# Performance work log

Measured on AMD Instinct MI355X. Metric: run time of the kernel, lower is better.

## Reference

```python
import jax, jax.numpy as jnp
import numpy as np

N, E, K, H, F_IN, F_OUT, Q = 50000, 1600000, 4, 4, 32, 32, 1


def setup_inputs() -> dict:
    key = jax.random.key(0)
    ks = jax.random.split(key, 5)
    x = jax.random.normal(ks[0], (N, H, F_IN, Q), dtype=jnp.float32)
    edge_index = jax.random.randint(ks[1], (2, E), 0, N, dtype=jnp.int64)
    edge_weight = jax.random.uniform(ks[2], (E,), dtype=jnp.float32)
    stdv = 1.0 / np.sqrt(F_IN * K)
    weight = jax.random.uniform(ks[3], (K, H, F_IN, F_OUT), dtype=jnp.float32, minval=-stdv, maxval=stdv)
    bias = jax.random.uniform(ks[4], (F_OUT,), dtype=jnp.float32, minval=-stdv, maxval=stdv)
    return {"x": x, "edge_index": edge_index, "edge_weight": edge_weight, "weight": weight, "bias": bias}


def reference(x, edge_index, edge_weight, weight, bias):
    # x: (n, h, f, q); weight: (K, h, f, g); edge_index: (2, E)
    n = x.shape[0]
    row, col = edge_index[0], edge_index[1]
    # remove_self_loops: zero out self-loop edges (static shapes, same math)
    mask = row != col
    ew = jnp.where(mask, edge_weight, jnp.zeros((), x.dtype))
    deg = jax.ops.segment_sum(mask.astype(x.dtype), row, num_segments=n)
    dinv = jnp.where(deg > 0, deg ** -0.5, jnp.zeros((), x.dtype))
    lap = -dinv[row] * ew * dinv[col]  # (E,)

    def spmm(t):
        # out[row] += lap * t[col]; t: (n, h, f, q)
        return jax.ops.segment_sum(lap[:, None, None, None] * t[col], row, num_segments=n)

    Kk = weight.shape[0]
    Tx0 = x
    out = jnp.einsum('nhfq,hfg->ngq', Tx0, weight[0])
    Tx1 = spmm(Tx0)
    out = out + jnp.einsum('nhfq,hfg->ngq', Tx1, weight[1])
    for k in range(2, Kk):
        Tx2 = 2.0 * spmm(Tx1) - Tx0
        out = out + jnp.einsum('nhfq,hfg->ngq', Tx2, weight[k])
        Tx0, Tx1 = Tx1, Tx2
    out = out[:, None]  # (n, 1, g, q) per collapse_H unsqueeze
    out = out + bias.reshape(1, 1, -1, 1)
    return out
```

## Files before the change

### kernel.cpp

```cpp
#include <hip/hip_runtime.h>


#define FEAT 128
#define GOUT 32
#define SCB 256
#define WPB 8
#define CH 4096
#define WCAP 16384
#define CAP 12032
#define TROW 160

typedef unsigned int uint;
typedef unsigned short ushort;

__device__ __forceinline__ ushort f2bf(float f) {
    uint u = __float_as_uint(f);
    return (ushort)((u + 0x7fffu + ((u >> 16) & 1u)) >> 16);
}
__device__ __forceinline__ float bflo(uint u) { return __uint_as_float(u << 16); }
__device__ __forceinline__ float bfhi(uint u) { return __uint_as_float(u & 0xffff0000u); }
__device__ __forceinline__ int tidx(int i) { return i + ((i >> 4) << 2); }

__global__ __launch_bounds__(1024) void bin_kernel(
    const int* __restrict__ ei, const float* __restrict__ ew, int E,
    int* __restrict__ bucketCursor, uint2* __restrict__ staging) {
    __shared__ int hist[256];
    __shared__ int base[256];
    int e0 = blockIdx.x * CH;
    int e1 = min(e0 + CH, E);
    int t = threadIdx.x;
    if (t < 256) hist[t] = 0;
    __syncthreads();
    for (int e = e0 + t; e < e1; e += 1024) {
        int r = ei[e], c = ei[(size_t)E + e];
        if (r != c) atomicAdd(&hist[r >> 8], 1);
    }
    __syncthreads();
    if (t < 256) {
        int h = hist[t];
        if (h > 0) {
            int run = atomicAdd(&bucketCursor[t], h);
            base[t] = t * CAP + run;
        }
        hist[t] = 0;
    }
    __syncthreads();
    for (int e = e0 + t; e < e1; e += 1024) {
        int r = ei[e], c = ei[(size_t)E + e];
        if (r == c) continue;
        float w = ew[e];
        int bk = r >> 8;
        int j = atomicAdd(&hist[bk], 1);
        int idx = base[bk] + j;
        if (idx < (bk + 1) * CAP)
            staging[idx] = make_uint2(__float_as_uint(w), ((uint)c << 16) | (uint)(r & 255));
    }
}

__global__ __launch_bounds__(256) void bucket_count_kernel(
    const uint2* __restrict__ staging, const int* __restrict__ bucketCursor,
    int* __restrict__ cnt, int n) {
    __shared__ int hist[256];
    int b = blockIdx.x;
    int t = threadIdx.x;
    hist[t] = 0;
    __syncthreads();
    int nrec = bucketCursor[b];
    const uint2* src = staging + (size_t)b * CAP;
    for (int k = t; k < nrec; k += 256)
        atomicAdd(&hist[src[k].y & 255], 1);
    __syncthreads();
    int r = (b << 8) + t;
    if (r < n) cnt[r] = hist[t];
}

__global__ void scan1_kernel(const int* __restrict__ cnt, int* __restrict__ partial,
                             int* __restrict__ blockSums, float* __restrict__ dinv, int n) {
    __shared__ int buf[2][SCB];
    int t = threadIdx.x;
    int i = blockIdx.x * SCB + t;
    int v = (i < n) ? cnt[i] : 0;
    if (i < n) dinv[i] = (v > 0) ? rsqrtf((float)v) : 0.0f;
    buf[0][t] = v;
    __syncthreads();
    int src = 0;
    for (int off = 1; off < SCB; off <<= 1) {
        int d = src ^ 1;
        buf[d][t] = buf[src][t] + ((t >= off) ? buf[src][t - off] : 0);
        __syncthreads();
        src = d;
    }
    int incl = buf[src][t];
    if (i < n) partial[i] = incl - v;
    if (t == SCB - 1) blockSums[blockIdx.x] = incl;
}

__global__ void scan2_kernel(const int* __restrict__ blockSums, int* __restrict__ blockOffsets,
                             int nb, int* __restrict__ total_out) {
    __shared__ int buf[2][SCB];
    __shared__ int carry_s;
    if (threadIdx.x == 0) carry_s = 0;
    __syncthreads();
    for (int base = 0; base < nb; base += SCB) {
        int i = base + (int)threadIdx.x;
        int v = (i < nb) ? blockSums[i] : 0;
        buf[0][threadIdx.x] = v;
        __syncthreads();
        int src = 0;
        for (int off = 1; off < SCB; off <<= 1) {
            int d = src ^ 1;
            buf[d][threadIdx.x] = buf[src][threadIdx.x] +
                                  ((threadIdx.x >= (unsigned)off) ? buf[src][threadIdx.x - off] : 0);
            __syncthreads();
            src = d;
        }
        int incl = buf[src][threadIdx.x];
        int c = carry_s;
        if (i < nb) blockOffsets[i] = c + incl - v;
        __syncthreads();
        if (threadIdx.x == SCB - 1) carry_s = c + incl;
        __syncthreads();
    }
    if (threadIdx.x == 0) *total_out = carry_s;
}

__global__ void scan3_kernel(const int* __restrict__ partial, const int* __restrict__ blockOffsets,
                             int* __restrict__ offsets, int n) {
    int i = blockIdx.x * blockDim.x + threadIdx.x;
    if (i < n) offsets[i] = partial[i] + blockOffsets[i / SCB];
}

__global__ __launch_bounds__(256) void scatter_kernel(
    const uint2* __restrict__ staging, const int* __restrict__ bucketCursor,
    const int* __restrict__ offsets, const float* __restrict__ dinv,
    uint* __restrict__ csr, int n) {
    __shared__ uint win[WCAP];
    __shared__ int roff[256];
    __shared__ int rcur[256];
    __shared__ float dloc[256];
    int b = blockIdx.x;
    int r0 = b << 8;
    int nrows = min(256, n - r0);
    int t = threadIdx.x;
    if (t < nrows) {
        roff[t] = offsets[r0 + t];
        dloc[t] = dinv[r0 + t];
    }
    rcur[t] = 0;
    __syncthreads();
    int wbeg = roff[0];
    int nrec = bucketCursor[b];
    bool fit = (nrec <= WCAP);
    const uint2* src = staging + (size_t)b * CAP;
    for (int k = t; k < nrec; k += 256) {
        uint2 rec = src[k];
        int col = rec.y >> 16;
        int rl = rec.y & 255;
        float lap = -dloc[rl] * __uint_as_float(rec.x) * dinv[col];
        uint colap = ((uint)col << 16) | (uint)f2bf(lap);
        int pos = roff[rl] + atomicAdd(&rcur[rl], 1);
        if (fit) win[pos - wbeg] = colap;
        else csr[pos] = colap;
    }
    __syncthreads();
    if (fit)
        for (int k = t; k < nrec; k += 256) csr[wbeg + k] = win[k];
}

__global__ __launch_bounds__(256) void cvt_einsum0_kernel(
    const float* __restrict__ x, ushort* __restrict__ xb,
    const float* __restrict__ W0, const float* __restrict__ bias,
    float* __restrict__ out, int n) {
    __shared__ __align__(16) float4 sW4[FEAT * GOUT / 4];
    __shared__ __align__(16) float sT[8 * TROW];
    const float* sW = (const float*)sW4;
    int t = threadIdx.x;
    const float4* wsrc = (const float4*)W0;
    for (int idx = t; idx < FEAT * GOUT / 4; idx += 256) sW4[idx] = wsrc[idx];
    size_t gi = (size_t)blockIdx.x * (8 * FEAT) + (size_t)t * 4;
    float4 v = make_float4(0.f, 0.f, 0.f, 0.f);
    bool inb = gi < (size_t)n * FEAT;
    if (inb) {
        v = *(const float4*)(x + gi);
        ushort4 o;
        o.x = f2bf(v.x); o.y = f2bf(v.y); o.z = f2bf(v.z); o.w = f2bf(v.w);
        *(ushort4*)(xb + gi) = o;
    }
    int nl = t >> 5;
    int f0 = 4 * (t & 31);
    *(float4*)&sT[nl * TROW + tidx(f0)] = v;
    __syncthreads();
    int l32 = t & 31;
    int q = l32 & 7;
    int part = l32 >> 3;
    float4 a4 = make_float4(0.f, 0.f, 0.f, 0.f);
#pragma unroll
    for (int j = 0; j < 8; ++j) {
        float4 t4 = *(const float4*)&sT[nl * TROW + tidx(part * 32 + 4 * j)];
        const float* wv0 = &sW[(part * 32 + 4 * j) * GOUT + 4 * q];
        float4 w0 = *(const float4*)(wv0);
        float4 w1 = *(const float4*)(wv0 + GOUT);
        float4 w2 = *(const float4*)(wv0 + 2 * GOUT);
        float4 w3 = *(const float4*)(wv0 + 3 * GOUT);
        a4.x += t4.x * w0.x + t4.y * w1.x + t4.z * w2.x + t4.w * w3.x;
        a4.y += t4.x * w0.y + t4.y * w1.y + t4.z * w2.y + t4.w * w3.y;
        a4.z += t4.x * w0.z + t4.y * w1.z + t4.z * w2.z + t4.w * w3.z;
        a4.w += t4.x * w0.w + t4.y * w1.w + t4.z * w2.w + t4.w * w3.w;
    }
    a4.x += __shfl_down(a4.x, 8);  a4.y += __shfl_down(a4.y, 8);
    a4.z += __shfl_down(a4.z, 8);  a4.w += __shfl_down(a4.w, 8);
    a4.x += __shfl_down(a4.x, 16); a4.y += __shfl_down(a4.y, 16);
    a4.z += __shfl_down(a4.z, 16); a4.w += __shfl_down(a4.w, 16);
    int node = blockIdx.x * 8 + nl;
    if (part == 0 && node < n) {
        const float4 b4 = *(const float4*)(bias + 4 * q);
        float4 r;
        r.x = a4.x + b4.x; r.y = a4.y + b4.y; r.z = a4.z + b4.z; r.w = a4.w + b4.w;
        *(float4*)(out + (size_t)node * GOUT + 4 * q) = r;
    }
}

__global__ __launch_bounds__(512) void spmm_fused_kernel(
    const ushort* __restrict__ inb, const ushort* __restrict__ sub,
    ushort* __restrict__ outb, const int* __restrict__ offsets,
    const uint* __restrict__ csr, const float* __restrict__ Wk,
    float* __restrict__ out, int n, int has_sub) {
    __shared__ __align__(16) float4 sW4[FEAT * GOUT / 4];
    __shared__ __align__(16) float sT[WPB][TROW];
    const float* sW = (const float*)sW4;
    int w = threadIdx.x >> 6;
    int lane = threadIdx.x & 63;
    int node = blockIdx.x * WPB + w;
    const float4* wsrc = (const float4*)Wk;
    for (int idx = threadIdx.x; idx < FEAT * GOUT / 4; idx += 512) sW4[idx] = wsrc[idx];
    float ox = 0.f, oy = 0.f;
    if (node < n) {
        int beg = offsets[node], end = offsets[node + 1];
        float ax = 0.f, ay = 0.f;
        int j = beg;
        for (; j + 8 <= end; j += 8) {
            uint q[8], u[8];
#pragma unroll
            for (int k = 0; k < 8; ++k) q[k] = __builtin_nontemporal_load(csr + j + k);
#pragma unroll
            for (int k = 0; k < 8; ++k)
                u[k] = ((const uint*)(inb + (size_t)(q[k] >> 16) * FEAT))[lane];
#pragma unroll
            for (int k = 0; k < 8; ++k) {
                float l = bflo(q[k]);
                ax += l * bflo(u[k]);
                ay += l * bfhi(u[k]);
            }
        }
        for (; j < end; ++j) {
            uint qe = __builtin_nontemporal_load(csr + j);
            uint u = ((const uint*)(inb + (size_t)(qe >> 16) * FEAT))[lane];
            float l = bflo(qe);
            ax += l * bflo(u);
            ay += l * bfhi(u);
        }
        ox = ax; oy = ay;
        if (has_sub) {
            uint s = __builtin_nontemporal_load((const uint*)(sub + (size_t)node * FEAT) + lane);
            ox = 2.f * ax - bflo(s);
            oy = 2.f * ay - bfhi(s);
        }
        uint o = (uint)f2bf(ox) | ((uint)f2bf(oy) << 16);
        __builtin_nontemporal_store(o, (uint*)(outb + (size_t)node * FEAT) + lane);
    }
    *(float2*)&sT[w][tidx(2 * lane)] = make_float2(ox, oy);
    __syncthreads();
    int q = lane & 7;
    int part = lane >> 3;
    float4 a4 = make_float4(0.f, 0.f, 0.f, 0.f);
#pragma unroll
    for (int j = 0; j < 4; ++j) {
        float4 t4 = *(const float4*)&sT[w][20 * part + 4 * j];
        const float* wv0 = &sW[(part * 16 + 4 * j) * GOUT + 4 * q];
        float4 w0 = *(const float4*)(wv0);
        float4 w1 = *(const float4*)(wv0 + GOUT);
        float4 w2 = *(const float4*)(wv0 + 2 * GOUT);
        float4 w3 = *(const float4*)(wv0 + 3 * GOUT);
        a4.x += t4.x * w0.x + t4.y * w1.x + t4.z * w2.x + t4.w * w3.x;
        a4.y += t4.x * w0.y + t4.y * w1.y + t4.z * w2.y + t4.w * w3.y;
        a4.z += t4.x * w0.z + t4.y * w1.z + t4.z * w2.z + t4.w * w3.z;
        a4.w += t4.x * w0.w + t4.y * w1.w + t4.z * w2.w + t4.w * w3.w;
    }
#pragma unroll
    for (int off = 8; off < 64; off <<= 1) {
        a4.x += __shfl_down(a4.x, off);
        a4.y += __shfl_down(a4.y, off);
        a4.z += __shfl_down(a4.z, off);
        a4.w += __shfl_down(a4.w, off);
    }
    if (part == 0 && node < n) {
        float4* po = (float4*)(out + (size_t)node * GOUT + 4 * q);
        float4 cur = *po;
        cur.x += a4.x; cur.y += a4.y; cur.z += a4.z; cur.w += a4.w;
        *po = cur;
    }
}

extern "C" void kernel_launch(void* const* d_in, const int* in_sizes, int n_in,
                              void* d_out, int out_size, void* d_ws, size_t ws_size,
                              hipStream_t stream) {
    const float* x = (const float*)d_in[0];
    const int* ei = (const int*)d_in[1];
    const float* ew = (const float*)d_in[2];
    const float* W = (const float*)d_in[3];
    const float* bias = (const float*)d_in[4];
    float* out = (float*)d_out;

    const int N = in_sizes[0] / FEAT;
    const int E = in_sizes[1] / 2;
    const int NB = (N + SCB - 1) / SCB;
    const int NBUK = (N + 255) >> 8;

    char* p = (char*)d_ws;
    auto alloc = [&](size_t bytes) {
        char* q = p;
        p += (bytes + 255) & ~(size_t)255;
        return q;
    };
    int* cnt = (int*)alloc((size_t)N * 4);
    int* offsets = (int*)alloc(((size_t)N + 1) * 4);
    float* dinv = (float*)alloc((size_t)N * 4);
    int* partial = (int*)alloc((size_t)N * 4);
    int* blockSums = (int*)alloc((size_t)NB * 4);
    int* blockOffsets = (int*)alloc((size_t)NB * 4);
    int* bucketCursor = (int*)alloc((size_t)NBUK * 4);
    uint* csr = (uint*)alloc((size_t)E * 4);
    ushort* xb = (ushort*)alloc((size_t)N * FEAT * 2);
    ushort* Ab = (ushort*)alloc((size_t)N * FEAT * 2);
    ushort* Bb = (ushort*)alloc((size_t)N * FEAT * 2);
    uint2* staging = (uint2*)Ab;
    (void)ws_size;

    hipMemsetAsync(bucketCursor, 0, (size_t)NBUK * 4, stream);

    bin_kernel<<<(E + CH - 1) / CH, 1024, 0, stream>>>(ei, ew, E, bucketCursor, staging);
    bucket_count_kernel<<<NBUK, 256, 0, stream>>>(staging, bucketCursor, cnt, N);
    scan1_kernel<<<NB, SCB, 0, stream>>>(cnt, partial, blockSums, dinv, N);
    scan2_kernel<<<1, SCB, 0, stream>>>(blockSums, blockOffsets, NB, offsets + N);
    scan3_kernel<<<NB, SCB, 0, stream>>>(partial, blockOffsets, offsets, N);
    scatter_kernel<<<NBUK, 256, 0, stream>>>(staging, bucketCursor, offsets, dinv, csr, N);

    cvt_einsum0_kernel<<<(N + 7) / 8, 256, 0, stream>>>(x, xb, W, bias, out, N);

    int sg = (N + WPB - 1) / WPB;
    spmm_fused_kernel<<<sg, 512, 0, stream>>>(xb, nullptr, Ab, offsets, csr,
                                              W + 1 * FEAT * GOUT, out, N, 0);
    spmm_fused_kernel<<<sg, 512, 0, stream>>>(Ab, xb, Bb, offsets, csr,
                                              W + 2 * FEAT * GOUT, out, N, 1);
    spmm_fused_kernel<<<sg, 512, 0, stream>>>(Bb, Ab, Ab, offsets, csr,
                                              W + 3 * FEAT * GOUT, out, N, 1);
}
```

Baseline: 407.4 us.

## Split features into 32-wide chunks for SpMM with per-chunk einsum atomics

New measurement: 384.1 us. 1.06x faster.

```diff
diff --git a/kernel.cpp b/kernel.cpp
--- a/kernel.cpp
+++ b/kernel.cpp
@@ -3,8 +3,9 @@
 
 #define FEAT 128
 #define GOUT 32
+#define NCH 4
+#define CHF 32
 #define SCB 256
-#define WPB 8
 #define CH 4096
 #define WCAP 16384
 #define CAP 12032
@@ -177,17 +178,17 @@
     int t = threadIdx.x;
     const float4* wsrc = (const float4*)W0;
     for (int idx = t; idx < FEAT * GOUT / 4; idx += 256) sW4[idx] = wsrc[idx];
-    size_t gi = (size_t)blockIdx.x * (8 * FEAT) + (size_t)t * 4;
+    int node = blockIdx.x * 8 + (t >> 5);
+    int f0 = 4 * (t & 31);
     float4 v = make_float4(0.f, 0.f, 0.f, 0.f);
-    bool inb = gi < (size_t)n * FEAT;
-    if (inb) {
-        v = *(const float4*)(x + gi);
+    if (node < n) {
+        v = *(const float4*)(x + (size_t)node * FEAT + f0);
         ushort4 o;
         o.x = f2bf(v.x); o.y = f2bf(v.y); o.z = f2bf(v.z); o.w = f2bf(v.w);
-        *(ushort4*)(xb + gi) = o;
+        int j0 = f0 >> 5;
+        *(ushort4*)(xb + ((size_t)j0 * n + node) * CHF + (f0 & 31)) = o;
     }
     int nl = t >> 5;
-    int f0 = 4 * (t & 31);
     *(float4*)&sT[nl * TROW + tidx(f0)] = v;
     __syncthreads();
     int l32 = t & 31;
@@ -211,7 +212,6 @@
     a4.z += __shfl_down(a4.z, 8);  a4.w += __shfl_down(a4.w, 8);
     a4.x += __shfl_down(a4.x, 16); a4.y += __shfl_down(a4.y, 16);
     a4.z += __shfl_down(a4.z, 16); a4.w += __shfl_down(a4.w, 16);
-    int node = blockIdx.x * 8 + nl;
     if (part == 0 && node < n) {
         const float4 b4 = *(const float4*)(bias + 4 * q);
         float4 r;
@@ -220,84 +220,68 @@
     }
 }
 
-__global__ __launch_bounds__(512) void spmm_fused_kernel(
+__global__ __launch_bounds__(512) void spmm_chunk_kernel(
     const ushort* __restrict__ inb, const ushort* __restrict__ sub,
     ushort* __restrict__ outb, const int* __restrict__ offsets,
     const uint* __restrict__ csr, const float* __restrict__ Wk,
-    float* __restrict__ out, int n, int has_sub) {
-    __shared__ __align__(16) float4 sW4[FEAT * GOUT / 4];
-    __shared__ __align__(16) float sT[WPB][TROW];
-    const float* sW = (const float*)sW4;
-    int w = threadIdx.x >> 6;
-    int lane = threadIdx.x & 63;
-    int node = blockIdx.x * WPB + w;
-    const float4* wsrc = (const float4*)Wk;
-    for (int idx = threadIdx.x; idx < FEAT * GOUT / 4; idx += 512) sW4[idx] = wsrc[idx];
-    float ox = 0.f, oy = 0.f;
+    float* __restrict__ out, int n, int has_sub, int nbj) {
+    __shared__ __align__(16) float sW[CHF * GOUT];
+    __shared__ float sT2[8][4][CHF];
+    int j = blockIdx.x / nbj;
+    int b = blockIdx.x % nbj;
+    int t = threadIdx.x;
+    const float4* wsrc = (const float4*)(Wk + j * CHF * GOUT);
+    for (int i2 = t; i2 < CHF * GOUT / 4; i2 += 512) ((float4*)sW)[i2] = wsrc[i2];
+    int w = t >> 6, lane = t & 63, s = lane >> 4, u = lane & 15;
+    int node = b * 32 + w * 4 + s;
+    int beg = 0, deg = 0;
+    if (node < n) { beg = offsets[node]; deg = offsets[node + 1] - beg; }
+    int m = deg;
+    m = max(m, __shfl_xor(m, 16));
+    m = max(m, __shfl_xor(m, 32));
+    const uint* inb_u = (const uint*)inb;
+    size_t jbase = (size_t)j * n * 16;
+    float tax = 0.f, tay = 0.f;
+    for (int it = 0; it < m; it += 4) {
+        uint q[4], uu[4];
+#pragma unroll
+        for (int k = 0; k < 4; ++k) {
+            int idx = it + k;
+            q[k] = (idx < deg) ? csr[beg + idx] : 0u;
+        }
+#pragma unroll
+        for (int k = 0; k < 4; ++k)
+            uu[k] = inb_u[jbase + (size_t)(q[k] >> 16) * 16 + u];
+#pragma unroll
+        for (int k = 0; k < 4; ++k) {
+            float l = bflo(q[k]);
+            tax += l * bflo(uu[k]);
+            tay += l * bfhi(uu[k]);
+        }
+    }
+    float ox = tax, oy = tay;
     if (node < n) {
-        int beg = offsets[node], end = offsets[node + 1];
-        float ax = 0.f, ay = 0.f;
-        int j = beg;
-        for (; j + 8 <= end; j += 8) {
-            uint q[8], u[8];
-#pragma unroll
-            for (int k = 0; k < 8; ++k) q[k] = __builtin_nontemporal_load(csr + j + k);
-#pragma unroll
-            for (int k = 0; k < 8; ++k)
-                u[k] = ((const uint*)(inb + (size_t)(q[k] >> 16) * FEAT))[lane];
-#pragma unroll
-            for (int k = 0; k < 8; ++k) {
-                float l = bflo(q[k]);
-                ax += l * bflo(u[k]);
-                ay += l * bfhi(u[k]);
-            }
-        }
-        for (; j < end; ++j) {
-            uint qe = __builtin_nontemporal_load(csr + j);
-            uint u = ((const uint*)(inb + (size_t)(qe >> 16) * FEAT))[lane];
-            float l = bflo(qe);
-            ax += l * bflo(u);
-            ay += l * bfhi(u);
-        }
-        ox = ax; oy = ay;
+        size_t base = jbase + (size_t)node * 16 + u;
         if (has_sub) {
-            uint s = __builtin_nontemporal_load((const uint*)(sub + (size_t)node * FEAT) + lane);
-            ox = 2.f * ax - bflo(s);
-            oy = 2.f * ay - bfhi(s);
-        }
-        uint o = (uint)f2bf(ox) | ((uint)f2bf(oy) << 16);
-        __builtin_nontemporal_store(o, (uint*)(outb + (size_t)node * FEAT) + lane);
-    }
-    *(float2*)&sT[w][tidx(2 * lane)] = make_float2(ox, oy);
-    __syncthreads();
-    int q = lane & 7;
-    int part = lane >> 3;
-    float4 a4 = make_float4(0.f, 0.f, 0.f, 0.f);
-#pragma unroll
-    for (int j = 0; j < 4; ++j) {
-        float4 t4 = *(const float4*)&sT[w][20 * part + 4 * j];
-        const float* wv0 = &sW[(part * 16 + 4 * j) * GOUT + 4 * q];
-        float4 w0 = *(const float4*)(wv0);
-        float4 w1 = *(const float4*)(wv0 + GOUT);
-        float4 w2 = *(const float4*)(wv0 + 2 * GOUT);
-        float4 w3 = *(const float4*)(wv0 + 3 * GOUT);
-        a4.x += t4.x * w0.x + t4.y * w1.x + t4.z * w2.x + t4.w * w3.x;
-        a4.y += t4.x * w0.y + t4.y * w1.y + t4.z * w2.y + t4.w * w3.y;
-        a4.z += t4.x * w0.z + t4.y * w1.z + t4.z * w2.z + t4.w * w3.z;
-        a4.w += t4.x * w0.w + t4.y * w1.w + t4.z * w2.w + t4.w * w3.w;
-    }
-#pragma unroll
-    for (int off = 8; off < 64; off <<= 1) {
-        a4.x += __shfl_down(a4.x, off);
-        a4.y += __shfl_down(a4.y, off);
-        a4.z += __shfl_down(a4.z, off);
-        a4.w += __shfl_down(a4.w, off);
-    }
-    if (part == 0 && node < n) {
-        float4* po = (float4*)(out + (size_t)node * GOUT + 4 * q);
-        float4 cur = *po;
-        cur.x += a4.x; cur.y += a4.y; cur.z += a4.z; cur.w += a4.w;
-        *po = cur;
+            uint sv = ((const uint*)sub)[base];
+            ox = 2.f * tax - bflo(sv);
+            oy = 2.f * tay - bfhi(sv);
+        }
+        ((uint*)outb)[base] = (uint)f2bf(ox) | ((uint)f2bf(oy) << 16);
+    }
+    sT2[w][s][2 * u] = ox;
+    sT2[w][s][2 * u + 1] = oy;
+    __syncthreads();
+    float a0 = 0.f, a1 = 0.f;
+#pragma unroll
+    for (int i = 0; i < CHF; ++i) {
+        float tv = sT2[w][s][i];
+        a0 += tv * sW[i * GOUT + u];
+        a1 += tv * sW[i * GOUT + u + 16];
+    }
+    if (node < n) {
+        atomicAdd(&out[(size_t)node * GOUT + u], a0);
+        atomicAdd(&out[(size_t)node * GOUT + u + 16], a1);
     }
 }
 
@@ -315,6 +299,7 @@
     const int E = in_sizes[1] / 2;
     const int NB = (N + SCB - 1) / SCB;
     const int NBUK = (N + 255) >> 8;
+    const int NBJ = (((N + 31) / 32 + 7) / 8) * 8;
 
     char* p = (char*)d_ws;
     auto alloc = [&](size_t bytes) {
@@ -329,7 +314,7 @@
     int* blockSums = (int*)alloc((size_t)NB * 4);
     int* blockOffsets = (int*)alloc((size_t)NB * 4);
     int* bucketCursor = (int*)alloc((size_t)NBUK * 4);
-    uint* csr = (uint*)alloc((size_t)E * 4);
+    uint* csr = (uint*)alloc(((size_t)E + 64) * 4);
     ushort* xb = (ushort*)alloc((size_t)N * FEAT * 2);
     ushort* Ab = (ushort*)alloc((size_t)N * FEAT * 2);
     ushort* Bb = (ushort*)alloc((size_t)N * FEAT * 2);
@@ -347,11 +332,11 @@
 
     cvt_einsum0_kernel<<<(N + 7) / 8, 256, 0, stream>>>(x, xb, W, bias, out, N);
 
-    int sg = (N + WPB - 1) / WPB;
-    spmm_fused_kernel<<<sg, 512, 0, stream>>>(xb, nullptr, Ab, offsets, csr,
-                                              W + 1 * FEAT * GOUT, out, N, 0);
-    spmm_fused_kernel<<<sg, 512, 0, stream>>>(Ab, xb, Bb, offsets, csr,
-                                              W + 2 * FEAT * GOUT, out, N, 1);
-    spmm_fused_kernel<<<sg, 512, 0, stream>>>(Bb, Ab, Ab, offsets, csr,
-                                              W + 3 * FEAT * GOUT, out, N, 1);
-}
+    dim3 sg(NCH * NBJ);
+    spmm_chunk_kernel<<<sg, 512, 0, stream>>>(xb, nullptr, Ab, offsets, csr,
+                                              W + 1 * FEAT * GOUT, out, N, 0, NBJ);
+    spmm_chunk_kernel<<<sg, 512, 0, stream>>>(Ab, xb, Bb, offsets, csr,
+                                              W + 2 * FEAT * GOUT, out, N, 1, NBJ);
+    spmm_chunk_kernel<<<sg, 512, 0, stream>>>(Bb, Ab, Ab, offsets, csr,
+                                              W + 3 * FEAT * GOUT, out, N, 1, NBJ);
+}
```
